# Kernel tuning notes

Measured on AMD Instinct MI355X. Metric: run time of the kernel, lower is better.

The kernel has to match this reference:

```python
import jax, jax.numpy as jnp
import numpy as np

HEADS = 16
EMBED_SIZE = 1024
HEAD_OUT = EMBED_SIZE // HEADS  # 64
B, T = 4, 2048


def setup_inputs() -> dict:
    key = jax.random.key(0)
    ks = jax.random.split(key, 7)
    std = 0.02
    return {
        "embeddings": jax.random.normal(ks[0], (B, T, EMBED_SIZE), dtype=jnp.float32),
        "Wq": jax.random.normal(ks[1], (HEAD_OUT, EMBED_SIZE), dtype=jnp.float32) * std,
        "bq": jax.random.normal(ks[2], (HEAD_OUT,), dtype=jnp.float32) * std,
        "Wk": jax.random.normal(ks[3], (HEAD_OUT, EMBED_SIZE), dtype=jnp.float32) * std,
        "bk": jax.random.normal(ks[4], (HEAD_OUT,), dtype=jnp.float32) * std,
        "Wv": jax.random.normal(ks[5], (HEAD_OUT, EMBED_SIZE), dtype=jnp.float32) * std,
        "bv": jax.random.normal(ks[6], (HEAD_OUT,), dtype=jnp.float32) * std,
    }


def reference(embeddings, Wq, bq, Wk, bk, Wv, bv):
    b, t, c = embeddings.shape
    x = embeddings.reshape(b * t, c)  # (BT, C) - original flattens batch+seq
    q = x @ Wq.T + bq  # (BT, head_out)
    k = x @ Wk.T + bk
    v = x @ Wv.T + bv
    scale = jnp.asarray(c, dtype=x.dtype) ** 0.5  # scaled by embed_size, not head_dim
    att = jax.nn.softmax((q @ k.T) / scale, axis=-1)  # (BT, BT) cross-batch attention
    y = (att @ v).reshape(b, t, -1)  # (B, T, head_out)
    # Every head uses the same shared q/k/v Linear, so all head outputs are identical;
    # the original loop concatenates the same result HEADS times.
    return jnp.tile(y, (1, 1, HEADS))  # (B, T, C)
```

## Files before the change

### kernel.cpp

```cpp
#include <hip/hip_runtime.h>
#include <stdint.h>

#define TOK 8192
#define EMB 1024
#define HD 64
#define HEADS 16
#define KVBLK 64

typedef float f32x4 __attribute__((ext_vector_type(4)));
typedef short s16x8 __attribute__((ext_vector_type(8)));

__device__ __forceinline__ unsigned short f2bf(float f) {
    unsigned u = __float_as_uint(f);
    unsigned r = (u + 0x7FFFu + ((u >> 16) & 1u)) >> 16;
    return (unsigned short)r;
}

__device__ __forceinline__ unsigned cvt_pk_bf16(float lo, float hi) {
    unsigned r;
    asm("v_cvt_pk_bf16_f32 %0, %1, %2" : "=v"(r) : "v"(lo), "v"(hi));
    return r;
}

__device__ __forceinline__ s16x8 frag4(unsigned a, unsigned b, unsigned c, unsigned d) {
    int4 t = make_int4((int)a, (int)b, (int)c, (int)d);
    return __builtin_bit_cast(s16x8, t);
}

__global__ __launch_bounds__(256) void prep_kernel(
        const float* __restrict__ Wq, const float* __restrict__ bq,
        const float* __restrict__ Wk, const float* __restrict__ bk,
        const float* __restrict__ Wv, const float* __restrict__ bv,
        unsigned short* __restrict__ wb, float* __restrict__ bb) {
    int gid = blockIdx.x * 256 + threadIdx.x;
    int row = gid >> 10, col = gid & 1023;
    const float QS = 1.4426950408889634f / 32.0f;
    float w;
    if (row < 64)       w = Wq[row * 1024 + col] * QS;
    else if (row < 128) w = Wk[(row - 64) * 1024 + col];
    else                w = Wv[(row - 128) * 1024 + col];
    wb[gid] = f2bf(w);
    if (gid < 192) {
        float b;
        if (gid < 64)       b = bq[gid] * QS;
        else if (gid < 128) b = bk[gid - 64];
        else                b = bv[gid - 128];
        bb[gid] = b;
    }
}

#define XPAD 1040
__global__ __launch_bounds__(768) void proj_kernel(
        const float* __restrict__ x, const unsigned short* __restrict__ wb,
        const float* __restrict__ bb,
        unsigned short* __restrict__ qw, unsigned char* __restrict__ kimg,
        unsigned char* __restrict__ vimg) {
    __shared__ __align__(16) unsigned short xb[16][XPAD];
    int tid = threadIdx.x;
    int row0 = blockIdx.x * 16;

    if (tid < 512) {
        #pragma unroll
        for (int i = 0; i < 8; ++i) {
            int flat = i * 2048 + tid * 4;
            int r = flat >> 10, col = flat & 1023;
            float4 f = *(const float4*)(x + (size_t)(row0 + r) * EMB + col);
            uint2 p;
            p.x = cvt_pk_bf16(f.x, f.y);
            p.y = cvt_pk_bf16(f.z, f.w);
            *(uint2*)(&xb[r][col]) = p;
        }
    }
    __syncthreads();

    int wave = tid >> 6;
    int lane = tid & 63;
    int c = lane & 15, g = lane >> 4;

    f32x4 acc0 = {}, acc1 = {};
    const unsigned short* bp0 = wb + (size_t)(wave * 16 + c) * EMB;
    #pragma unroll 8
    for (int ks = 0; ks < 16; ++ks) {
        s16x8 a0 = *(const s16x8*)(&xb[c][ks * 32 + g * 8]);
        s16x8 b0 = *(const s16x8*)(bp0 + ks * 32 + g * 8);
        acc0 = __builtin_amdgcn_mfma_f32_16x16x32_bf16(a0, b0, acc0, 0, 0, 0);
        s16x8 a1 = *(const s16x8*)(&xb[c][(ks + 16) * 32 + g * 8]);
        s16x8 b1 = *(const s16x8*)(bp0 + (ks + 16) * 32 + g * 8);
        acc1 = __builtin_amdgcn_mfma_f32_16x16x32_bf16(a1, b1, acc1, 0, 0, 0);
    }
    float bias = bb[wave * 16 + c];
    f32x4 acc;
    acc[0] = acc0[0] + acc1[0] + bias;
    acc[1] = acc0[1] + acc1[1] + bias;
    acc[2] = acc0[2] + acc1[2] + bias;
    acc[3] = acc0[3] + acc1[3] + bias;

    size_t tile = (size_t)(row0 >> 6);
    int tI = (row0 >> 4) & 3;

    if (wave < 4) {
        int col = wave * 16 + c;
        #pragma unroll
        for (int r = 0; r < 4; ++r)
            qw[(size_t)(row0 + g * 4 + r) * HD + col] = f2bf(acc[r]);
    } else if (wave < 8) {
        int wv = wave - 4;
        int C = wv * 16 + c;
        int kh = C >> 5;
        int gg = (C & 31) >> 3;
        int j = C & 7;
        unsigned char* base = kimg + tile * 8192 + (size_t)((kh * 4 + tI) * 1024 + j * 2);
        #pragma unroll
        for (int r = 0; r < 4; ++r) {
            int cl = g * 4 + r;
            *(unsigned short*)(base + (gg * 16 + cl) * 16) = f2bf(acc[r]);
        }
    } else {
        int t = wave - 8;
        int base16 = tI * 16 + g * 4;
        int ks = base16 >> 5;
        int s = (base16 >> 3) & 3;
        int gg = ((s & 1) << 1) | (s >> 1);
        int j0 = base16 & 7;
        uint2 pack;
        pack.x = cvt_pk_bf16(acc[0], acc[1]);
        pack.y = cvt_pk_bf16(acc[2], acc[3]);
        *(uint2*)(vimg + tile * 8192 +
                  (size_t)((ks * 4 + t) * 1024 + (gg * 16 + c) * 16 + j0 * 2)) = pack;
    }
}

template <int S>
__global__ __launch_bounds__(256, 3) void attn_kernel(
        const unsigned short* __restrict__ qw, const unsigned char* __restrict__ kimg,
        const unsigned char* __restrict__ vimg,
        float* __restrict__ po, float* __restrict__ pl) {
    constexpr int KVS = TOK / S;
    constexpr int NIT = KVS / KVBLK;
    constexpr int QB = TOK / 128;
    __shared__ __align__(16) unsigned char lds[2][16384];
    int wave = threadIdx.x >> 6;
    int lane = threadIdx.x & 63;
    int c = lane & 15, g = lane >> 4;
    int qb = blockIdx.x % QB;
    int split = blockIdx.x / QB;
    int wq0 = qb * 128 + wave * 32;
    int tile0 = split * NIT;
    bool odd = (g & 1) != 0;

    s16x8 aq[2][2];
    #pragma unroll
    for (int qt = 0; qt < 2; ++qt)
        #pragma unroll
        for (int kh = 0; kh < 2; ++kh)
            aq[qt][kh] = *(const s16x8*)(qw + (size_t)(wq0 + qt * 16 + c) * HD + kh * 32 + g * 8);

    f32x4 o[2][4] = {};
    float l[2] = {};

    auto stage = [&](int buf, int tile) {
        const unsigned char* kg = kimg + (size_t)tile * 8192;
        const unsigned char* vg = vimg + (size_t)tile * 8192;
        #pragma unroll
        for (int j = 0; j < 2; ++j) {
            int off = (j * 4 + wave) * 1024;
            __builtin_amdgcn_global_load_lds(
                (const __attribute__((address_space(1))) void*)(kg + off + lane * 16),
                (__attribute__((address_space(3))) void*)(&lds[buf][off]), 16, 0, 0);
            __builtin_amdgcn_global_load_lds(
                (const __attribute__((address_space(1))) void*)(vg + off + lane * 16),
                (__attribute__((address_space(3))) void*)(&lds[buf][8192 + off]), 16, 0, 0);
        }
    };

    stage(0, tile0);
    __syncthreads();

    int buf = 0;
    #pragma unroll 1
    for (int it = 0; it < NIT; ++it) {
        int nt = (it + 1 < NIT) ? it + 1 : it;
        stage(buf ^ 1, tile0 + nt);

        const unsigned char* Kl = &lds[buf][0];
        const unsigned char* Vl = &lds[buf][8192];

        s16x8 kf[2][4];
        #pragma unroll
        for (int kh = 0; kh < 2; ++kh)
            #pragma unroll
            for (int t = 0; t < 4; ++t)
                kf[kh][t] = *(const s16x8*)(Kl + (kh * 4 + t) * 1024 + lane * 16);

        f32x4 st[2][4] = {};
        #pragma unroll
        for (int kh = 0; kh < 2; ++kh)
            #pragma unroll
            for (int q = 0; q < 2; ++q)
                #pragma unroll
                for (int t = 0; t < 4; ++t)
                    st[q][t] = __builtin_amdgcn_mfma_f32_16x16x32_bf16(
                        kf[kh][t], aq[q][kh], st[q][t], 0, 0, 0);

        unsigned Wall[2][8];
        #pragma unroll
        for (int q = 0; q < 2; ++q) {
            float p[4][4];
            #pragma unroll
            for (int t = 0; t < 4; ++t)
                #pragma unroll
                for (int r = 0; r < 4; ++r)
                    p[t][r] = exp2f(st[q][t][r]);
            float s0 = (p[0][0] + p[0][1]) + (p[0][2] + p[0][3]);
            float s1 = (p[1][0] + p[1][1]) + (p[1][2] + p[1][3]);
            float s2 = (p[2][0] + p[2][1]) + (p[2][2] + p[2][3]);
            float s3 = (p[3][0] + p[3][1]) + (p[3][2] + p[3][3]);
            l[q] += (s0 + s1) + (s2 + s3);
            #pragma unroll
            for (int t = 0; t < 4; ++t) {
                Wall[q][t * 2 + 0] = cvt_pk_bf16(p[t][0], p[t][1]);
                Wall[q][t * 2 + 1] = cvt_pk_bf16(p[t][2], p[t][3]);
            }
        }

        #pragma unroll
        for (int ks = 0; ks < 2; ++ks) {
            s16x8 vf[4];
            #pragma unroll
            for (int t = 0; t < 4; ++t)
                vf[t] = *(const s16x8*)(Vl + (ks * 4 + t) * 1024 + lane * 16);
            #pragma unroll
            for (int qt = 0; qt < 2; ++qt) {
                unsigned ael = Wall[qt][4 * ks + 0], aeh = Wall[qt][4 * ks + 1];
                unsigned aol = Wall[qt][4 * ks + 2], aoh = Wall[qt][4 * ks + 3];
                unsigned sl = odd ? ael : aol;
                unsigned sh = odd ? aeh : aoh;
                unsigned rl = (unsigned)__builtin_amdgcn_ds_swizzle((int)sl, 0x401F);
                unsigned rh = (unsigned)__builtin_amdgcn_ds_swizzle((int)sh, 0x401F);
                unsigned f0 = odd ? rl : ael;
                unsigned f1 = odd ? rh : aeh;
                unsigned f2 = odd ? aol : rl;
                unsigned f3 = odd ? aoh : rh;
                s16x8 pa = frag4(f0, f1, f2, f3);
                #pragma unroll
                for (int t = 0; t < 4; ++t)
                    o[qt][t] = __builtin_amdgcn_mfma_f32_16x16x32_bf16(pa, vf[t], o[qt][t], 0, 0, 0);
            }
        }
        __syncthreads();
        buf ^= 1;
    }

    #pragma unroll
    for (int qt = 0; qt < 2; ++qt) {
        #pragma unroll
        for (int t = 0; t < 4; ++t)
            #pragma unroll
            for (int r = 0; r < 4; ++r)
                po[((size_t)split * TOK + wq0 + qt * 16 + g * 4 + r) * HD + t * 16 + c] = o[qt][t][r];
        float v = l[qt];
        v += __shfl_xor(v, 16);
        v += __shfl_xor(v, 32);
        if (g == 0)
            pl[split * TOK + wq0 + qt * 16 + c] = v;
    }
}

template <int S>
__global__ __launch_bounds__(256) void combine_kernel(
        const float* __restrict__ po, const float* __restrict__ pl,
        float* __restrict__ out) {
    int gid = blockIdx.x * 256 + threadIdx.x;
    int row = gid >> 4;
    int dc = (gid & 15) * 4;
    float4 acc = {0.f, 0.f, 0.f, 0.f};
    float denom = 0.f;
    #pragma unroll
    for (int s = 0; s < S; ++s) {
        denom += pl[s * TOK + row];
        float4 p = *(const float4*)(po + ((size_t)s * TOK + row) * HD + dc);
        acc.x += p.x; acc.y += p.y; acc.z += p.z; acc.w += p.w;
    }
    float inv = 1.0f / denom;
    acc.x *= inv; acc.y *= inv; acc.z *= inv; acc.w *= inv;
    #pragma unroll
    for (int h = 0; h < HEADS; ++h)
        *(float4*)(out + (size_t)row * EMB + h * HD + dc) = acc;
}

extern "C" void kernel_launch(void* const* d_in, const int* in_sizes, int n_in,
                              void* d_out, int out_size, void* d_ws, size_t ws_size,
                              hipStream_t stream) {
    const float* x  = (const float*)d_in[0];
    const float* Wq = (const float*)d_in[1];
    const float* bq = (const float*)d_in[2];
    const float* Wk = (const float*)d_in[3];
    const float* bk = (const float*)d_in[4];
    const float* Wv = (const float*)d_in[5];
    const float* bv = (const float*)d_in[6];
    float* out = (float*)d_out;
    char* ws = (char*)d_ws;
    unsigned short* wb   = (unsigned short*)(ws + 0x000000);
    float*          bb   = (float*)         (ws + 0x060000);
    unsigned short* qw   = (unsigned short*)(ws + 0x061000);
    unsigned char*  kimg = (unsigned char*) (ws + 0x161000);
    unsigned char*  vimg = (unsigned char*) (ws + 0x261000);
    float*          po   = (float*)         (ws + 0x361000);

    prep_kernel<<<dim3(768), dim3(256), 0, stream>>>(Wq, bq, Wk, bk, Wv, bv, wb, bb);
    proj_kernel<<<dim3(512), dim3(768), 0, stream>>>(x, wb, bb, qw, kimg, vimg);

    const size_t base = 0x361000;
    const size_t per_split = (size_t)TOK * HD * 4;
    const size_t per_pl    = (size_t)TOK * 4;
    auto need = [&](int s) { return base + (size_t)s * (per_split + per_pl); };

    if (ws_size >= need(16)) {
        float* pl = (float*)(ws + base + 16 * per_split);
        attn_kernel<16><<<dim3(64 * 16), dim3(256), 0, stream>>>(qw, kimg, vimg, po, pl);
        combine_kernel<16><<<dim3(512), dim3(256), 0, stream>>>(po, pl, out);
    } else {
        float* pl = (float*)(ws + base + 8 * per_split);
        attn_kernel<8><<<dim3(64 * 8), dim3(256), 0, stream>>>(qw, kimg, vimg, po, pl);
        combine_kernel<8><<<dim3(512), dim3(256), 0, stream>>>(po, pl, out);
    }
}
```

Baseline: 151.2 us.

## Shrink KV tile to 32 keys with new K/V layouts, drop swizzle, raise occupancy

Halves the KV block per iteration from 64 to 32 keys and rewrites the K and V image layouts written by the projection kernel so the P fragment maps straight onto the MFMA A operand, which removes the ds_swizzle exchange. LDS per block is halved and launch bounds are raised to 4 blocks per CU. The change also uses the hardware exp2 builtin and raises wave priority around the MFMA sections. The cost is twice as many loop iterations and barriers, with less work per barrier available to hide load latency.

```diff
diff --git a/kernel.cpp b/kernel.cpp
--- a/kernel.cpp
+++ b/kernel.cpp
@@ -5,7 +5,6 @@
 #define EMB 1024
 #define HD 64
 #define HEADS 16
-#define KVBLK 64
 
 typedef float f32x4 __attribute__((ext_vector_type(4)));
 typedef short s16x8 __attribute__((ext_vector_type(8)));
@@ -95,8 +94,8 @@
     acc[2] = acc0[2] + acc1[2] + bias;
     acc[3] = acc0[3] + acc1[3] + bias;
 
-    size_t tile = (size_t)(row0 >> 6);
-    int tI = (row0 >> 4) & 3;
+    size_t tile32 = (size_t)(row0 >> 5);
+    int tI2 = (row0 >> 4) & 1;
 
     if (wave < 4) {
         int col = wave * 16 + c;
@@ -104,41 +103,36 @@
         for (int r = 0; r < 4; ++r)
             qw[(size_t)(row0 + g * 4 + r) * HD + col] = f2bf(acc[r]);
     } else if (wave < 8) {
-        int wv = wave - 4;
-        int C = wv * 16 + c;
+        int C = (wave - 4) * 16 + c;
         int kh = C >> 5;
         int gg = (C & 31) >> 3;
         int j = C & 7;
-        unsigned char* base = kimg + tile * 8192 + (size_t)((kh * 4 + tI) * 1024 + j * 2);
+        unsigned char* base = kimg + tile32 * 4096 +
+                              (size_t)((kh * 2 + tI2) * 1024 + j * 2);
         #pragma unroll
         for (int r = 0; r < 4; ++r) {
             int cl = g * 4 + r;
             *(unsigned short*)(base + (gg * 16 + cl) * 16) = f2bf(acc[r]);
         }
     } else {
-        int t = wave - 8;
-        int base16 = tI * 16 + g * 4;
-        int ks = base16 >> 5;
-        int s = (base16 >> 3) & 3;
-        int gg = ((s & 1) << 1) | (s >> 1);
-        int j0 = base16 & 7;
+        int td = wave - 8;
         uint2 pack;
         pack.x = cvt_pk_bf16(acc[0], acc[1]);
         pack.y = cvt_pk_bf16(acc[2], acc[3]);
-        *(uint2*)(vimg + tile * 8192 +
-                  (size_t)((ks * 4 + t) * 1024 + (gg * 16 + c) * 16 + j0 * 2)) = pack;
+        *(uint2*)(vimg + tile32 * 4096 +
+                  (size_t)(td * 1024 + (g * 16 + c) * 16 + tI2 * 8)) = pack;
     }
 }
 
 template <int S>
-__global__ __launch_bounds__(256, 3) void attn_kernel(
+__global__ __launch_bounds__(256, 4) void attn_kernel(
         const unsigned short* __restrict__ qw, const unsigned char* __restrict__ kimg,
         const unsigned char* __restrict__ vimg,
         float* __restrict__ po, float* __restrict__ pl) {
     constexpr int KVS = TOK / S;
-    constexpr int NIT = KVS / KVBLK;
+    constexpr int NIT = KVS / 32;
     constexpr int QB = TOK / 128;
-    __shared__ __align__(16) unsigned char lds[2][16384];
+    __shared__ __align__(16) unsigned char lds[2][8192];
     int wave = threadIdx.x >> 6;
     int lane = threadIdx.x & 63;
     int c = lane & 15, g = lane >> 4;
@@ -146,7 +140,6 @@
     int split = blockIdx.x / QB;
     int wq0 = qb * 128 + wave * 32;
     int tile0 = split * NIT;
-    bool odd = (g & 1) != 0;
 
     s16x8 aq[2][2];
     #pragma unroll
@@ -159,18 +152,14 @@
     float l[2] = {};
 
     auto stage = [&](int buf, int tile) {
-        const unsigned char* kg = kimg + (size_t)tile * 8192;
-        const unsigned char* vg = vimg + (size_t)tile * 8192;
-        #pragma unroll
-        for (int j = 0; j < 2; ++j) {
-            int off = (j * 4 + wave) * 1024;
-            __builtin_amdgcn_global_load_lds(
-                (const __attribute__((address_space(1))) void*)(kg + off + lane * 16),
-                (__attribute__((address_space(3))) void*)(&lds[buf][off]), 16, 0, 0);
-            __builtin_amdgcn_global_load_lds(
-                (const __attribute__((address_space(1))) void*)(vg + off + lane * 16),
-                (__attribute__((address_space(3))) void*)(&lds[buf][8192 + off]), 16, 0, 0);
-        }
+        const unsigned char* kg = kimg + (size_t)tile * 4096;
+        const unsigned char* vg = vimg + (size_t)tile * 4096;
+        __builtin_amdgcn_global_load_lds(
+            (const __attribute__((address_space(1))) void*)(kg + wave * 1024 + lane * 16),
+            (__attribute__((address_space(3))) void*)(&lds[buf][wave * 1024]), 16, 0, 0);
+        __builtin_amdgcn_global_load_lds(
+            (const __attribute__((address_space(1))) void*)(vg + wave * 1024 + lane * 16),
+            (__attribute__((address_space(3))) void*)(&lds[buf][4096 + wave * 1024]), 16, 0, 0);
     };
 
     stage(0, tile0);
@@ -183,70 +172,54 @@
         stage(buf ^ 1, tile0 + nt);
 
         const unsigned char* Kl = &lds[buf][0];
-        const unsigned char* Vl = &lds[buf][8192];
-
-        s16x8 kf[2][4];
-        #pragma unroll
-        for (int kh = 0; kh < 2; ++kh)
+        const unsigned char* Vl = &lds[buf][4096];
+
+        f32x4 st[2][2] = {};
+        __builtin_amdgcn_s_setprio(1);
+        #pragma unroll
+        for (int kh = 0; kh < 2; ++kh) {
+            s16x8 kf0 = *(const s16x8*)(Kl + (kh * 2 + 0) * 1024 + lane * 16);
+            s16x8 kf1 = *(const s16x8*)(Kl + (kh * 2 + 1) * 1024 + lane * 16);
             #pragma unroll
-            for (int t = 0; t < 4; ++t)
-                kf[kh][t] = *(const s16x8*)(Kl + (kh * 4 + t) * 1024 + lane * 16);
-
-        f32x4 st[2][4] = {};
-        #pragma unroll
-        for (int kh = 0; kh < 2; ++kh)
+            for (int q = 0; q < 2; ++q) {
+                st[q][0] = __builtin_amdgcn_mfma_f32_16x16x32_bf16(kf0, aq[q][kh], st[q][0], 0, 0, 0);
+                st[q][1] = __builtin_amdgcn_mfma_f32_16x16x32_bf16(kf1, aq[q][kh], st[q][1], 0, 0, 0);
+            }
+        }
+        __builtin_amdgcn_s_setprio(0);
+
+        unsigned Wall[2][4];
+        #pragma unroll
+        for (int q = 0; q < 2; ++q) {
+            float p[2][4];
             #pragma unroll
-            for (int q = 0; q < 2; ++q)
-                #pragma unroll
-                for (int t = 0; t < 4; ++t)
-                    st[q][t] = __builtin_amdgcn_mfma_f32_16x16x32_bf16(
-                        kf[kh][t], aq[q][kh], st[q][t], 0, 0, 0);
-
-        unsigned Wall[2][8];
-        #pragma unroll
-        for (int q = 0; q < 2; ++q) {
-            float p[4][4];
-            #pragma unroll
-            for (int t = 0; t < 4; ++t)
+            for (int t = 0; t < 2; ++t)
                 #pragma unroll
                 for (int r = 0; r < 4; ++r)
-                    p[t][r] = exp2f(st[q][t][r]);
+                    p[t][r] = __builtin_amdgcn_exp2f(st[q][t][r]);
             float s0 = (p[0][0] + p[0][1]) + (p[0][2] + p[0][3]);
             float s1 = (p[1][0] + p[1][1]) + (p[1][2] + p[1][3]);
-            float s2 = (p[2][0] + p[2][1]) + (p[2][2] + p[2][3]);
-            float s3 = (p[3][0] + p[3][1]) + (p[3][2] + p[3][3]);
-            l[q] += (s0 + s1) + (s2 + s3);
+            l[q] += s0 + s1;
+            Wall[q][0] = cvt_pk_bf16(p[0][0], p[0][1]);
+            Wall[q][1] = cvt_pk_bf16(p[0][2], p[0][3]);
+            Wall[q][2] = cvt_pk_bf16(p[1][0], p[1][1]);
+            Wall[q][3] = cvt_pk_bf16(p[1][2], p[1][3]);
+        }
+
+        s16x8 vf[4];
+        #pragma unroll
+        for (int td = 0; td < 4; ++td)
+            vf[td] = *(const s16x8*)(Vl + td * 1024 + lane * 16);
+        __builtin_amdgcn_s_setprio(1);
+        #pragma unroll
+        for (int q = 0; q < 2; ++q) {
+            s16x8 pa = frag4(Wall[q][0], Wall[q][1], Wall[q][2], Wall[q][3]);
             #pragma unroll
-            for (int t = 0; t < 4; ++t) {
-                Wall[q][t * 2 + 0] = cvt_pk_bf16(p[t][0], p[t][1]);
-                Wall[q][t * 2 + 1] = cvt_pk_bf16(p[t][2], p[t][3]);
-            }
-        }
-
-        #pragma unroll
-        for (int ks = 0; ks < 2; ++ks) {
-            s16x8 vf[4];
-            #pragma unroll
-            for (int t = 0; t < 4; ++t)
-                vf[t] = *(const s16x8*)(Vl + (ks * 4 + t) * 1024 + lane * 16);
-            #pragma unroll
-            for (int qt = 0; qt < 2; ++qt) {
-                unsigned ael = Wall[qt][4 * ks + 0], aeh = Wall[qt][4 * ks + 1];
-                unsigned aol = Wall[qt][4 * ks + 2], aoh = Wall[qt][4 * ks + 3];
-                unsigned sl = odd ? ael : aol;
-                unsigned sh = odd ? aeh : aoh;
-                unsigned rl = (unsigned)__builtin_amdgcn_ds_swizzle((int)sl, 0x401F);
-                unsigned rh = (unsigned)__builtin_amdgcn_ds_swizzle((int)sh, 0x401F);
-                unsigned f0 = odd ? rl : ael;
-                unsigned f1 = odd ? rh : aeh;
-                unsigned f2 = odd ? aol : rl;
-                unsigned f3 = odd ? aoh : rh;
-                s16x8 pa = frag4(f0, f1, f2, f3);
-                #pragma unroll
-                for (int t = 0; t < 4; ++t)
-                    o[qt][t] = __builtin_amdgcn_mfma_f32_16x16x32_bf16(pa, vf[t], o[qt][t], 0, 0, 0);
-            }
-        }
+            for (int td = 0; td < 4; ++td)
+                o[q][td] = __builtin_amdgcn_mfma_f32_16x16x32_bf16(pa, vf[td], o[q][td], 0, 0, 0);
+        }
+        __builtin_amdgcn_s_setprio(0);
+
         __syncthreads();
         buf ^= 1;
     }
@@ -254,10 +227,10 @@
     #pragma unroll
     for (int qt = 0; qt < 2; ++qt) {
         #pragma unroll
-        for (int t = 0; t < 4; ++t)
+        for (int td = 0; td < 4; ++td)
             #pragma unroll
             for (int r = 0; r < 4; ++r)
-                po[((size_t)split * TOK + wq0 + qt * 16 + g * 4 + r) * HD + t * 16 + c] = o[qt][t][r];
+                po[((size_t)split * TOK + wq0 + qt * 16 + g * 4 + r) * HD + td * 16 + c] = o[qt][td][r];
         float v = l[qt];
         v += __shfl_xor(v, 16);
         v += __shfl_xor(v, 32);
```

Measured after the change: 144.7 us. -4.3%, faster.
